# Kernel optimization log

Measured on AMD Instinct MI355X. Metric: run time of the kernel, lower is better.

## Reference

```python
import jax, jax.numpy as jnp
import numpy as np

B, S, D = 4, 4096, 2048
H, HD = 16, 128
TILE = 16
N_TILES = 8


def setup_inputs() -> dict:
    key = jax.random.key(0)
    ks = jax.random.split(key, 6)
    x = jax.random.normal(ks[0], (B, S, D), dtype=jnp.float32)
    anchor_indices = jax.random.randint(ks[1], (B, H, N_TILES), 0, S // TILE).astype(jnp.int32)
    sc = 1.0 / np.sqrt(D)
    Wq = jax.random.normal(ks[2], (D, H * HD), dtype=jnp.float32) * sc
    Wk = jax.random.normal(ks[3], (D, H * HD), dtype=jnp.float32) * sc
    Wv = jax.random.normal(ks[4], (D, H * HD), dtype=jnp.float32) * sc
    Wo = jax.random.normal(ks[5], (H * HD, D), dtype=jnp.float32) * (1.0 / np.sqrt(H * HD))
    return {"x": x, "anchor_indices": anchor_indices, "Wq": Wq, "Wk": Wk, "Wv": Wv, "Wo": Wo}


def reference(x, anchor_indices, Wq, Wk, Wv, Wo):
    batch, seq_len, _ = x.shape
    # QKV projections -> (b, h, s, d)
    q = (x @ Wq).reshape(batch, seq_len, H, HD).transpose(0, 2, 1, 3)
    k = (x @ Wk).reshape(batch, seq_len, H, HD).transpose(0, 2, 1, 3)
    v = (x @ Wv).reshape(batch, seq_len, H, HD).transpose(0, 2, 1, 3)
    # Force last tile slot to the current local tile (causal local attention)
    current_tile_idx = (seq_len - 1) // TILE
    tiles = anchor_indices.at[:, :, -1].set(current_tile_idx)
    # Expand tile indices to token indices: (b, h, n_tiles*TILE)
    token_indices = (tiles[..., None] * TILE + jnp.arange(TILE)[None, None, None, :]).reshape(batch, H, -1)
    # Gather sparse K/V per head: (b, h, K, d)
    k_sparse = jnp.take_along_axis(k, token_indices[..., None], axis=2)
    v_sparse = jnp.take_along_axis(v, token_indices[..., None], axis=2)
    logits = jnp.einsum('bhqd,bhkd->bhqk', q, k_sparse) / jnp.sqrt(jnp.float32(HD))
    # Causal mask over gathered (non-contiguous) key positions
    future_mask = token_indices[:, :, None, :] > jnp.arange(seq_len)[None, None, :, None]
    logits = jnp.where(future_mask, -1e10, logits)
    weights = jax.nn.softmax(logits, axis=-1)
    out = jnp.einsum('bhqk,bhkd->bhqd', weights, v_sparse)
    out = out.transpose(0, 2, 1, 3).reshape(batch, seq_len, H * HD)
    return out @ Wo
```

## Files before the change

### kernel.cpp

```cpp
#include <hip/hip_runtime.h>
#include <stdint.h>

#define Bz 4
#define Sz 4096
#define Dz 2048
#define Hz 16
#define HDz 128
#define NTz 8
#define TILEz 16

typedef __bf16 bf16x8 __attribute__((ext_vector_type(8)));
typedef float f32x4 __attribute__((ext_vector_type(4)));
typedef float fx4 __attribute__((ext_vector_type(4)));
typedef unsigned short u16;
typedef u16 u16x4 __attribute__((ext_vector_type(4)));
typedef u16 u16x8 __attribute__((ext_vector_type(8)));

#define MFMA16(a, b, c) __builtin_amdgcn_mfma_f32_16x16x32_bf16((a), (b), (c), 0, 0, 0)

__device__ __forceinline__ u16 f2bf(float f) {
    uint32_t u = __builtin_bit_cast(uint32_t, f);
    return (u16)((u + 0x7fffu + ((u >> 16) & 1u)) >> 16);
}

__device__ __forceinline__ void async16(const u16* g, u16* l) {
    __builtin_amdgcn_global_load_lds(
        (const __attribute__((address_space(1))) unsigned int*)(g),
        (__attribute__((address_space(3))) unsigned int*)(l), 16, 0, 0);
}

#define BAR()                                  \
    do {                                       \
        asm volatile("" ::: "memory");         \
        __builtin_amdgcn_s_barrier();          \
        asm volatile("" ::: "memory");         \
    } while (0)

__global__ void cvt_x(const float* __restrict__ x, u16* __restrict__ o) {
    int i = blockIdx.x * 256 + threadIdx.x;
    const fx4* xv = (const fx4*)x;
    fx4 a = xv[i * 2], b = xv[i * 2 + 1];
    u16x8 r;
    r[0] = f2bf(a[0]); r[1] = f2bf(a[1]); r[2] = f2bf(a[2]); r[3] = f2bf(a[3]);
    r[4] = f2bf(b[0]); r[5] = f2bf(b[1]); r[6] = f2bf(b[2]); r[7] = f2bf(b[3]);
    ((u16x8*)o)[i] = r;
}

__global__ void transpose_cvt(const float* W0, const float* W1, const float* W2, const float* W3,
                              u16* O0, u16* O1, u16* O2, u16* O3) {
    const float* W; u16* O;
    switch (blockIdx.z) {
        case 0: W = W0; O = O0; break;
        case 1: W = W1; O = O1; break;
        case 2: W = W2; O = O2; break;
        default: W = W3; O = O3; break;
    }
    __shared__ u16 tile[32][33];
    int bx = blockIdx.x * 32, by = blockIdx.y * 32;
    int tx = threadIdx.x, ty = threadIdx.y;
#pragma unroll
    for (int i = 0; i < 32; i += 8)
        tile[ty + i][tx] = f2bf(W[(long)(by + ty + i) * 2048 + bx + tx]);
    __syncthreads();
#pragma unroll
    for (int i = 0; i < 32; i += 8)
        O[(long)(bx + ty + i) * 2048 + by + tx] = tile[tx][ty + i];
}

__device__ __forceinline__ void stage2(const u16* s0, const u16* s1, u16* chunk, int w, int koff) {
    async16(s0 + koff, chunk + w * 512);
    async16(s1 + koff, chunk + w * 512 + 4096);
}

template <typename OutT>
__global__ __launch_bounds__(512, 2) void gemm256(const u16* __restrict__ A, const u16* __restrict__ BT,
                                                  OutT* __restrict__ C, int M_, int N_, int K_) {
    __shared__ __align__(1024) u16 lds[65536];
    const int t = threadIdx.x, w = t >> 6, l = t & 63, lr = l & 15, quad = l >> 4;
    const int wm = w >> 2, wn = w & 3;
    const int nbn = N_ >> 8;
    const int cpx = gridDim.x >> 3;
    const int swz = (blockIdx.x & 7) * cpx + (blockIdx.x >> 3);
    const int bm = swz / nbn, bn = swz % nbn;

    const u16* sA[2]; const u16* sB[2];
#pragma unroll
    for (int r = 0; r < 2; r++) {
        int idx = r * 512 + t;
        int row = idx >> 2;
        int q = (t & 3) ^ ((row >> 2) & 2);
        sA[r] = A + (long)(bm * 256 + row) * K_ + q * 8;
        sB[r] = BT + (long)(bn * 256 + row) * K_ + q * 8;
    }
    const int qro = (quad ^ (((lr >> 3) & 1) << 1)) * 8;
    const int rowA0 = wm * 128 + lr;
    const int rowB0 = wn * 64 + lr;
    const int nt = K_ >> 6;

    f32x4 acc[8][4] = {};

    stage2(sA[0], sA[1], lds + 0, w, 0);
    stage2(sB[0], sB[1], lds + 32768, w, 0);
    stage2(sA[0], sA[1], lds + 8192, w, 32);
    stage2(sB[0], sB[1], lds + 32768 + 8192, w, 32);
    const int k1 = (nt > 1) ? 64 : 0;
    stage2(sA[0], sA[1], lds + 16384, w, k1);
    stage2(sB[0], sB[1], lds + 32768 + 16384, w, k1);
    asm volatile("s_waitcnt vmcnt(4)" ::: "memory");
    BAR();

    for (int g = 0; g < nt; ++g) {
        const int cb = g & 1, ob = cb ^ 1;
        const int t1k = ((g + 1 < nt ? g + 1 : nt - 1) << 6) + 32;
        const int t2k = ((g + 2 < nt ? g + 2 : nt - 1) << 6);
        const u16* Abase = lds + cb * 16384;
        const u16* Bbase = lds + 32768 + cb * 16384;
#pragma unroll
        for (int kh = 0; kh < 2; ++kh) {
            const u16* Ach = Abase + kh * 8192;
            const u16* Bch = Bbase + kh * 8192;
            bf16x8 bfr[4];
#pragma unroll
            for (int j = 0; j < 4; ++j)
                bfr[j] = *(const bf16x8*)(Bch + (rowB0 + j * 16) * 32 + qro);
#pragma unroll
            for (int mh = 0; mh < 2; ++mh) {
                bf16x8 af[4];
#pragma unroll
                for (int i = 0; i < 4; ++i)
                    af[i] = *(const bf16x8*)(Ach + (rowA0 + mh * 64 + i * 16) * 32 + qro);
                if (kh == 0 && mh == 0)      stage2(sA[0], sA[1], lds + ob * 16384 + 8192, w, t1k);
                else if (kh == 0 && mh == 1) stage2(sB[0], sB[1], lds + 32768 + ob * 16384 + 8192, w, t1k);
                else if (kh == 1 && mh == 0) stage2(sA[0], sA[1], lds + cb * 16384, w, t2k);
                else                         stage2(sB[0], sB[1], lds + 32768 + cb * 16384, w, t2k);
                asm volatile("" ::: "memory");
                __builtin_amdgcn_s_barrier();
                asm volatile("s_waitcnt lgkmcnt(0)" ::: "memory");
                __builtin_amdgcn_s_setprio(1);
#pragma unroll
                for (int i = 0; i < 4; ++i)
#pragma unroll
                    for (int j = 0; j < 4; ++j)
                        acc[mh * 4 + i][j] = MFMA16(af[i], bfr[j], acc[mh * 4 + i][j]);
                __builtin_amdgcn_s_setprio(0);
                if (kh == 1 && mh == 1) asm volatile("s_waitcnt vmcnt(4)" ::: "memory");
                BAR();
            }
        }
    }

    const long crow0 = (long)bm * 256 + wm * 128;
    const int ccol0 = bn * 256 + wn * 64;
#pragma unroll
    for (int f = 0; f < 8; ++f) {
        long row0 = crow0 + (f >> 2) * 64 + (f & 3) * 16 + quad * 4;
#pragma unroll
        for (int j = 0; j < 4; ++j) {
            int col = ccol0 + j * 16 + lr;
#pragma unroll
            for (int rg = 0; rg < 4; ++rg) {
                long idx = (row0 + rg) * N_ + col;
                if constexpr (sizeof(OutT) == 2) ((u16*)C)[idx] = f2bf(acc[f][j][rg]);
                else ((float*)C)[idx] = acc[f][j][rg];
            }
        }
    }
}

#define KV_SPLIT 4
#define KV_CHUNK (Dz / KV_SPLIT)
__global__ __launch_bounds__(256) void kv_sparse(const u16* __restrict__ xbf, const u16* __restrict__ WkT,
                                                 const u16* __restrict__ WvT, const int* __restrict__ anchor,
                                                 float* __restrict__ part) {
    const int bh = blockIdx.x, which = blockIdx.y, split = blockIdx.z;
    const int b = bh >> 4, h = bh & 15;
    __shared__ int toks[128];
    __shared__ __align__(16) u16 As[4096];
    __shared__ __align__(16) u16 Bs[4096];
    const int t = threadIdx.x, w = t >> 6, l = t & 63, lr = l & 15, quad = l >> 4;
    if (t < 128) {
        int j = t >> 4;
        int tile = (j == 7) ? (Sz / TILEz - 1) : anchor[bh * NTz + j];
        toks[t] = tile * TILEz + (t & 15);
    }
    __syncthreads();
    const u16* gA[2]; const u16* gB[2]; u16* lA[2]; u16* lB[2];
#pragma unroll
    for (int r = 0; r < 2; r++) {
        int c = r * 256 + t;
        int row = c >> 2, col8 = (c & 3) * 8;
        const u16* xrow = xbf + ((long)b * Sz + toks[row]) * Dz + col8;
        const u16* wrowK = WkT + (long)(h * HDz + row) * Dz + col8;
        const u16* wrowV = WvT + (long)(h * HDz + row) * Dz + col8;
        gA[r] = (which == 0) ? xrow : wrowV;
        gB[r] = (which == 0) ? wrowK : xrow;
        lA[r] = &As[(r * 256 + w * 64) * 8];
        lB[r] = &Bs[(r * 256 + w * 64) * 8];
    }
    f32x4 acc[4][4] = {};
    const int wr = (w >> 1) * 64, wc = (w & 1) * 64;
    const int ks0 = split * KV_CHUNK;
    for (int k0 = ks0; k0 < ks0 + KV_CHUNK; k0 += 32) {
        async16(gA[0] + k0, lA[0]); async16(gA[1] + k0, lA[1]);
        async16(gB[0] + k0, lB[0]); async16(gB[1] + k0, lB[1]);
        __syncthreads();
        bf16x8 af[4], bfr[4];
#pragma unroll
        for (int i = 0; i < 4; i++) af[i] = *(const bf16x8*)&As[(wr + i * 16 + lr) * 32 + quad * 8];
#pragma unroll
        for (int j = 0; j < 4; j++) bfr[j] = *(const bf16x8*)&Bs[(wc + j * 16 + lr) * 32 + quad * 8];
#pragma unroll
        for (int i = 0; i < 4; i++)
#pragma unroll
            for (int j = 0; j < 4; j++) acc[i][j] = MFMA16(af[i], bfr[j], acc[i][j]);
        __syncthreads();
    }
    float* out = part + (((long)split * 2 + which) * 64 + bh) * 16384;
#pragma unroll
    for (int i = 0; i < 4; i++) {
        int row0 = wr + i * 16 + quad * 4;
#pragma unroll
        for (int j = 0; j < 4; j++) {
            int col = wc + j * 16 + lr;
#pragma unroll
            for (int rg = 0; rg < 4; rg++) out[(row0 + rg) * 128 + col] = acc[i][j][rg];
        }
    }
}

__global__ void kv_reduce(const float* __restrict__ part, u16* __restrict__ kv) {
    long i = ((long)blockIdx.x * 256 + threadIdx.x) * 4;
    const long stride = 2L * 64 * 16384;
    fx4 s = *(const fx4*)(part + i);
#pragma unroll
    for (int sp = 1; sp < KV_SPLIT; sp++) {
        fx4 p = *(const fx4*)(part + sp * stride + i);
        s[0] += p[0]; s[1] += p[1]; s[2] += p[2]; s[3] += p[3];
    }
    u16x4 r;
    r[0] = f2bf(s[0]); r[1] = f2bf(s[1]); r[2] = f2bf(s[2]); r[3] = f2bf(s[3]);
    *(u16x4*)(kv + i) = r;
}

__global__ __launch_bounds__(512) void attn_kernel(u16* QAO,
                                                   const u16* __restrict__ ksp, const u16* __restrict__ vspT,
                                                   const int* __restrict__ anchor) {
    const int st = blockIdx.x, h = blockIdx.y, b = blockIdx.z;
    const int bh = b * Hz + h, s0 = st * 128;
    __shared__ __align__(16) u16 Kl[16384];
    __shared__ __align__(16) u16 Ps[128 * 136];
    __shared__ int toks[128];
    const int t = threadIdx.x, w = t >> 6, l = t & 63, lr = l & 15, quad = l >> 4;
    if (t < 128) {
        int j = t >> 4;
        int tile = (j == 7) ? (Sz / TILEz - 1) : anchor[bh * NTz + j];
        toks[t] = tile * TILEz + (t & 15);
    }
    const u16* Qb = QAO + (long)(b * Sz + s0 + w * 16) * 2048 + h * HDz;
    const u16* Kb = ksp + (long)bh * HDz * 128;
    const u16* Vb = vspT + (long)bh * HDz * 128;
    bf16x8 qf[4];
#pragma unroll
    for (int ks = 0; ks < 4; ks++)
        qf[ks] = *(const bf16x8*)(Qb + (long)lr * 2048 + ks * 32 + quad * 8);
#pragma unroll
    for (int r = 0; r < 4; r++) {
        int idx = r * 512 + t;
        int row = idx >> 4, c = idx & 15;
        async16(Kb + row * 128 + ((c ^ (row & 7)) * 8), Kl + (r * 512 + w * 64) * 8);
    }
    __syncthreads();
    f32x4 acc[8] = {};
#pragma unroll
    for (int ks = 0; ks < 4; ks++) {
#pragma unroll
        for (int j = 0; j < 8; j++) {
            int kr = j * 16 + lr;
            bf16x8 bj = *(const bf16x8*)(Kl + kr * 128 + (((ks * 4 + quad) ^ (lr & 7)) * 8));
            acc[j] = MFMA16(qf[ks], bj, acc[j]);
        }
    }
    int tokj[8];
#pragma unroll
    for (int j = 0; j < 8; j++) tokj[j] = toks[j * 16 + lr];
    const float scale = 0.08838834764831845f;
#pragma unroll
    for (int rg = 0; rg < 4; rg++) {
        int qpos = s0 + w * 16 + quad * 4 + rg;
        float v[8];
#pragma unroll
        for (int j = 0; j < 8; j++)
            v[j] = (tokj[j] > qpos) ? -1e10f : acc[j][rg] * scale;
        float mx = v[0];
#pragma unroll
        for (int j = 1; j < 8; j++) mx = fmaxf(mx, v[j]);
        mx = fmaxf(mx, __shfl_xor(mx, 1, 64));
        mx = fmaxf(mx, __shfl_xor(mx, 2, 64));
        mx = fmaxf(mx, __shfl_xor(mx, 4, 64));
        mx = fmaxf(mx, __shfl_xor(mx, 8, 64));
        float s = 0.f;
#pragma unroll
        for (int j = 0; j < 8; j++) { v[j] = exp2f((v[j] - mx) * 1.4426950408889634f); s += v[j]; }
        s += __shfl_xor(s, 1, 64);
        s += __shfl_xor(s, 2, 64);
        s += __shfl_xor(s, 4, 64);
        s += __shfl_xor(s, 8, 64);
        float rs = 1.0f / s;
        int prow = w * 16 + quad * 4 + rg;
#pragma unroll
        for (int j = 0; j < 8; j++) Ps[prow * 136 + j * 16 + lr] = f2bf(v[j] * rs);
    }
    bf16x8 va[4];
#pragma unroll
    for (int ks = 0; ks < 4; ks++)
        va[ks] = *(const bf16x8*)(Vb + (w * 16 + lr) * 128 + ks * 32 + quad * 8);
    __syncthreads();
    f32x4 oacc[8] = {};
#pragma unroll
    for (int ks = 0; ks < 4; ks++) {
#pragma unroll
        for (int j = 0; j < 8; j++) {
            bf16x8 pj = *(const bf16x8*)&Ps[(j * 16 + lr) * 136 + ks * 32 + quad * 8];
            oacc[j] = MFMA16(va[ks], pj, oacc[j]);
        }
    }
#pragma unroll
    for (int j = 0; j < 8; j++) {
        u16x4 pk;
#pragma unroll
        for (int rg = 0; rg < 4; rg++) pk[rg] = f2bf(oacc[j][rg]);
        int d = w * 16 + quad * 4;
        int q = j * 16 + lr;
        *(u16x4*)(QAO + (long)(b * Sz + s0 + q) * 2048 + h * HDz + d) = pk;
    }
}

extern "C" void kernel_launch(void* const* d_in, const int* in_sizes, int n_in,
                              void* d_out, int out_size, void* d_ws, size_t ws_size,
                              hipStream_t stream) {
    const float* x = (const float*)d_in[0];
    const int* anchor = (const int*)d_in[1];
    const float* Wq = (const float*)d_in[2];
    const float* Wk = (const float*)d_in[3];
    const float* Wv = (const float*)d_in[4];
    const float* Wo = (const float*)d_in[5];

    char* ws = (char*)d_ws;
    const size_t XB = 67108864;
    const size_t WB = 8388608;
    u16* xbf = (u16*)(ws);
    u16* WqT = (u16*)(ws + XB);
    u16* WkT = (u16*)(ws + XB + WB);
    u16* WvT = (u16*)(ws + XB + 2 * WB);
    u16* WoT = (u16*)(ws + XB + 3 * WB);
    u16* Qb  = (u16*)(ws + XB + 4 * WB);
    float* kvpart = (float*)(ws + XB + 4 * WB);
    u16* ksp = (u16*)(ws + 2 * XB + 4 * WB);
    u16* vspT= (u16*)(ws + 2 * XB + 4 * WB + 2097152);

    cvt_x<<<16384, 256, 0, stream>>>(x, xbf);
    transpose_cvt<<<dim3(64, 64, 4), dim3(32, 8), 0, stream>>>(Wq, Wk, Wv, Wo, WqT, WkT, WvT, WoT);
    kv_sparse<<<dim3(64, 2, KV_SPLIT), 256, 0, stream>>>(xbf, WkT, WvT, anchor, kvpart);
    kv_reduce<<<2048, 256, 0, stream>>>(kvpart, ksp);
    gemm256<u16><<<dim3(512), dim3(512), 0, stream>>>(xbf, WqT, Qb, 16384, 2048, 2048);
    attn_kernel<<<dim3(32, 16, 4), dim3(512), 0, stream>>>(Qb, ksp, vspT, anchor);
    gemm256<float><<<dim3(512), dim3(512), 0, stream>>>(Qb, WoT, (float*)d_out, 16384, 2048, 2048);
}
```

Baseline: 600.8 us.

## Software-pipeline GEMM LDS fragment loads with MFMA and vectorize weight transpose

The GEMM main loop is restructured so LDS fragment reads for the next sub-step are issued before the current sub-step's MFMAs, using double-buffered register fragments and adjusted vmcnt waits. The goal is to hide LDS read latency behind matrix math instead of waiting on lgkmcnt before each MFMA block. The weight transpose-convert kernel now uses float4 loads and 4-wide u16 stores with a padded, aligned LDS tile. The change adds register pressure and makes the barrier and waitcnt ordering more fragile, since buffer reuse depends on the exact vmcnt counts.

```diff
diff --git a/kernel.cpp b/kernel.cpp
--- a/kernel.cpp
+++ b/kernel.cpp
@@ -55,16 +55,19 @@
         case 2: W = W2; O = O2; break;
         default: W = W3; O = O3; break;
     }
-    __shared__ u16 tile[32][33];
+    __shared__ __align__(16) u16 tile[32][36];
     int bx = blockIdx.x * 32, by = blockIdx.y * 32;
-    int tx = threadIdx.x, ty = threadIdx.y;
-#pragma unroll
-    for (int i = 0; i < 32; i += 8)
-        tile[ty + i][tx] = f2bf(W[(long)(by + ty + i) * 2048 + bx + tx]);
+    int tid = threadIdx.y * 32 + threadIdx.x;
+    int row = tid >> 3, c4 = tid & 7;
+    fx4 wv = *(const fx4*)&W[(long)(by + row) * 2048 + bx + c4 * 4];
+    u16x4 t4;
+    t4[0] = f2bf(wv[0]); t4[1] = f2bf(wv[1]); t4[2] = f2bf(wv[2]); t4[3] = f2bf(wv[3]);
+    *(u16x4*)&tile[row][c4 * 4] = t4;
     __syncthreads();
-#pragma unroll
-    for (int i = 0; i < 32; i += 8)
-        O[(long)(bx + ty + i) * 2048 + by + tx] = tile[tx][ty + i];
+    u16x4 o4;
+#pragma unroll
+    for (int c = 0; c < 4; ++c) o4[c] = tile[c4 * 4 + c][row];
+    *(u16x4*)&O[(long)(bx + row) * 2048 + by + c4 * 4] = o4;
 }
 
 __device__ __forceinline__ void stage2(const u16* s0, const u16* s1, u16* chunk, int w, int koff) {
@@ -98,6 +101,7 @@
     const int nt = K_ >> 6;
 
     f32x4 acc[8][4] = {};
+    bf16x8 bfr_a[4], bfr_b[4], af_a[4], af_b[4];
 
     stage2(sA[0], sA[1], lds + 0, w, 0);
     stage2(sB[0], sB[1], lds + 32768, w, 0);
@@ -106,47 +110,81 @@
     const int k1 = (nt > 1) ? 64 : 0;
     stage2(sA[0], sA[1], lds + 16384, w, k1);
     stage2(sB[0], sB[1], lds + 32768 + 16384, w, k1);
-    asm volatile("s_waitcnt vmcnt(4)" ::: "memory");
+    asm volatile("s_waitcnt vmcnt(8)" ::: "memory");
     BAR();
+#pragma unroll
+    for (int j = 0; j < 4; ++j) bfr_a[j] = *(const bf16x8*)(lds + 32768 + (rowB0 + j * 16) * 32 + qro);
+#pragma unroll
+    for (int i = 0; i < 4; ++i) af_a[i] = *(const bf16x8*)(lds + (rowA0 + i * 16) * 32 + qro);
+    asm volatile("s_waitcnt lgkmcnt(0)" ::: "memory");
+    __builtin_amdgcn_sched_barrier(0);
 
     for (int g = 0; g < nt; ++g) {
         const int cb = g & 1, ob = cb ^ 1;
         const int t1k = ((g + 1 < nt ? g + 1 : nt - 1) << 6) + 32;
         const int t2k = ((g + 2 < nt ? g + 2 : nt - 1) << 6);
-        const u16* Abase = lds + cb * 16384;
-        const u16* Bbase = lds + 32768 + cb * 16384;
-#pragma unroll
-        for (int kh = 0; kh < 2; ++kh) {
-            const u16* Ach = Abase + kh * 8192;
-            const u16* Bch = Bbase + kh * 8192;
-            bf16x8 bfr[4];
-#pragma unroll
-            for (int j = 0; j < 4; ++j)
-                bfr[j] = *(const bf16x8*)(Bch + (rowB0 + j * 16) * 32 + qro);
-#pragma unroll
-            for (int mh = 0; mh < 2; ++mh) {
-                bf16x8 af[4];
-#pragma unroll
-                for (int i = 0; i < 4; ++i)
-                    af[i] = *(const bf16x8*)(Ach + (rowA0 + mh * 64 + i * 16) * 32 + qro);
-                if (kh == 0 && mh == 0)      stage2(sA[0], sA[1], lds + ob * 16384 + 8192, w, t1k);
-                else if (kh == 0 && mh == 1) stage2(sB[0], sB[1], lds + 32768 + ob * 16384 + 8192, w, t1k);
-                else if (kh == 1 && mh == 0) stage2(sA[0], sA[1], lds + cb * 16384, w, t2k);
-                else                         stage2(sB[0], sB[1], lds + 32768 + cb * 16384, w, t2k);
-                asm volatile("" ::: "memory");
-                __builtin_amdgcn_s_barrier();
-                asm volatile("s_waitcnt lgkmcnt(0)" ::: "memory");
-                __builtin_amdgcn_s_setprio(1);
-#pragma unroll
-                for (int i = 0; i < 4; ++i)
-#pragma unroll
-                    for (int j = 0; j < 4; ++j)
-                        acc[mh * 4 + i][j] = MFMA16(af[i], bfr[j], acc[mh * 4 + i][j]);
-                __builtin_amdgcn_s_setprio(0);
-                if (kh == 1 && mh == 1) asm volatile("s_waitcnt vmcnt(4)" ::: "memory");
-                BAR();
-            }
-        }
+        const u16* Acb = lds + cb * 16384;
+        const u16* Bcb = lds + 32768 + cb * 16384;
+        const u16* Anx = lds + ob * 16384;
+        const u16* Bnx = lds + 32768 + ob * 16384;
+
+#pragma unroll
+        for (int i = 0; i < 4; ++i) af_b[i] = *(const bf16x8*)(Acb + (rowA0 + 64 + i * 16) * 32 + qro);
+        stage2(sA[0], sA[1], (u16*)(lds + ob * 16384 + 8192), w, t1k);
+        __builtin_amdgcn_s_setprio(1);
+#pragma unroll
+        for (int i = 0; i < 4; ++i)
+#pragma unroll
+            for (int j = 0; j < 4; ++j) acc[i][j] = MFMA16(af_a[i], bfr_a[j], acc[i][j]);
+        __builtin_amdgcn_s_setprio(0);
+        asm volatile("s_waitcnt lgkmcnt(0)" ::: "memory");
+        __builtin_amdgcn_sched_barrier(0);
+        asm volatile("s_waitcnt vmcnt(6)" ::: "memory");
+        BAR();
+
+#pragma unroll
+        for (int j = 0; j < 4; ++j) bfr_b[j] = *(const bf16x8*)(Bcb + 8192 + (rowB0 + j * 16) * 32 + qro);
+#pragma unroll
+        for (int i = 0; i < 4; ++i) af_a[i] = *(const bf16x8*)(Acb + 8192 + (rowA0 + i * 16) * 32 + qro);
+        stage2(sB[0], sB[1], (u16*)(lds + 32768 + ob * 16384 + 8192), w, t1k);
+        __builtin_amdgcn_s_setprio(1);
+#pragma unroll
+        for (int i = 0; i < 4; ++i)
+#pragma unroll
+            for (int j = 0; j < 4; ++j) acc[4 + i][j] = MFMA16(af_b[i], bfr_a[j], acc[4 + i][j]);
+        __builtin_amdgcn_s_setprio(0);
+        asm volatile("s_waitcnt lgkmcnt(0)" ::: "memory");
+        __builtin_amdgcn_sched_barrier(0);
+        BAR();
+
+#pragma unroll
+        for (int i = 0; i < 4; ++i) af_b[i] = *(const bf16x8*)(Acb + 8192 + (rowA0 + 64 + i * 16) * 32 + qro);
+        stage2(sA[0], sA[1], (u16*)(lds + cb * 16384), w, t2k);
+        __builtin_amdgcn_s_setprio(1);
+#pragma unroll
+        for (int i = 0; i < 4; ++i)
+#pragma unroll
+            for (int j = 0; j < 4; ++j) acc[i][j] = MFMA16(af_a[i], bfr_b[j], acc[i][j]);
+        __builtin_amdgcn_s_setprio(0);
+        asm volatile("s_waitcnt lgkmcnt(0)" ::: "memory");
+        __builtin_amdgcn_sched_barrier(0);
+        asm volatile("s_waitcnt vmcnt(6)" ::: "memory");
+        BAR();
+
+#pragma unroll
+        for (int j = 0; j < 4; ++j) bfr_a[j] = *(const bf16x8*)(Bnx + (rowB0 + j * 16) * 32 + qro);
+#pragma unroll
+        for (int i = 0; i < 4; ++i) af_a[i] = *(const bf16x8*)(Anx + (rowA0 + i * 16) * 32 + qro);
+        stage2(sB[0], sB[1], (u16*)(lds + 32768 + cb * 16384), w, t2k);
+        __builtin_amdgcn_s_setprio(1);
+#pragma unroll
+        for (int i = 0; i < 4; ++i)
+#pragma unroll
+            for (int j = 0; j < 4; ++j) acc[4 + i][j] = MFMA16(af_b[i], bfr_b[j], acc[4 + i][j]);
+        __builtin_amdgcn_s_setprio(0);
+        asm volatile("s_waitcnt lgkmcnt(0)" ::: "memory");
+        __builtin_amdgcn_sched_barrier(0);
+        BAR();
     }
 
     const long crow0 = (long)bm * 256 + wm * 128;
```

New measurement: 601.8 us. Within noise of the previous version (+0.2%).
